# Performance work log

Hardware: AMD Instinct MI355X
Metric: run time of the kernel (lower is better)

Reference implementation:

```python
import jax, jax.numpy as jnp
import numpy as np

N_NODES = 50000
N_EDGES = 800000
IN_F = 129
HID = 32
HEADS = 4
N_CLS = 40
NEG_SLOPE = 0.2
BN_EPS = 1e-5


def setup_inputs() -> dict:
    key = jax.random.key(0)
    ks = jax.random.split(key, 16)
    x = jax.random.normal(ks[0], (N_NODES, IN_F), dtype=jnp.float32)
    edge_index = jax.random.randint(ks[1], (2, N_EDGES), 0, N_NODES, dtype=jnp.int64)
    # BatchNorm1d (eval mode: running stats)
    bn_gamma = jax.random.normal(ks[2], (IN_F,), dtype=jnp.float32) * 0.1 + 1.0
    bn_beta = jax.random.normal(ks[3], (IN_F,), dtype=jnp.float32) * 0.1
    bn_mean = jax.random.normal(ks[4], (IN_F,), dtype=jnp.float32) * 0.1
    bn_var = jax.random.uniform(ks[5], (IN_F,), dtype=jnp.float32, minval=0.5, maxval=1.5)
    # GATConv 1: in=129 -> heads*hid
    s1 = 1.0 / np.sqrt(IN_F)
    W1 = jax.random.uniform(ks[6], (IN_F, HEADS * HID), dtype=jnp.float32, minval=-s1, maxval=s1)
    a1_src = jax.random.uniform(ks[7], (HEADS, HID), dtype=jnp.float32, minval=-s1, maxval=s1)
    a1_dst = jax.random.uniform(ks[8], (HEADS, HID), dtype=jnp.float32, minval=-s1, maxval=s1)
    b1 = jnp.zeros((HEADS * HID,), dtype=jnp.float32)
    # GATConv 2: in=heads*hid -> heads*n_cls (concat=True default)
    in2 = HEADS * HID
    s2 = 1.0 / np.sqrt(in2)
    W2 = jax.random.uniform(ks[9], (in2, HEADS * N_CLS), dtype=jnp.float32, minval=-s2, maxval=s2)
    a2_src = jax.random.uniform(ks[10], (HEADS, N_CLS), dtype=jnp.float32, minval=-s2, maxval=s2)
    a2_dst = jax.random.uniform(ks[11], (HEADS, N_CLS), dtype=jnp.float32, minval=-s2, maxval=s2)
    b2 = jnp.zeros((HEADS * N_CLS,), dtype=jnp.float32)
    return {"x": x, "edge_index": edge_index,
            "bn_gamma": bn_gamma, "bn_beta": bn_beta, "bn_mean": bn_mean, "bn_var": bn_var,
            "W1": W1, "a1_src": a1_src, "a1_dst": a1_dst, "b1": b1,
            "W2": W2, "a2_src": a2_src, "a2_dst": a2_dst, "b2": b2}


def gat_conv(x, W, a_src, a_dst, bias, src, dst, num_nodes, heads, out_ch):
    # h: [N, H, C]
    h = (x @ W).reshape(num_nodes, heads, out_ch)
    alpha_s = jnp.einsum('nhc,hc->nh', h, a_src)   # [N, H]
    alpha_d = jnp.einsum('nhc,hc->nh', h, a_dst)   # [N, H]
    e = alpha_s[src] + alpha_d[dst]                # [E, H]
    e = jnp.where(e > 0, e, NEG_SLOPE * e)         # LeakyReLU
    # segment softmax grouped by destination node
    e_max = jax.ops.segment_max(e, dst, num_segments=num_nodes)
    p = jnp.exp(e - e_max[dst])
    denom = jax.ops.segment_sum(p, dst, num_segments=num_nodes)
    alpha = p / denom[dst]                         # [E, H]
    msg = h[src] * alpha[:, :, None]               # [E, H, C]
    out = jax.ops.segment_sum(msg, dst, num_segments=num_nodes)
    return out.reshape(num_nodes, heads * out_ch) + bias


def reference(x, edge_index, bn_gamma, bn_beta, bn_mean, bn_var,
              W1, a1_src, a1_dst, b1, W2, a2_src, a2_dst, b2):
    N = x.shape[0]
    loops = jnp.arange(N, dtype=edge_index.dtype)
    src = jnp.concatenate([edge_index[0], loops])  # add self loops (PyG default)
    dst = jnp.concatenate([edge_index[1], loops])
    # BatchNorm1d eval; dropout is identity in eval
    h = (x - bn_mean) * jax.lax.rsqrt(bn_var + BN_EPS) * bn_gamma + bn_beta
    h = gat_conv(h, W1, a1_src, a1_dst, b1, src, dst, N, HEADS, HID)
    h = jax.nn.elu(h)
    h = gat_conv(h, W2, a2_src, a2_dst, b2, src, dst, N, HEADS, N_CLS)
    return h
```

## Files before the change

### kernel.cpp

```cpp
#include <hip/hip_runtime.h>

#define N_NODES 50000
#define N_EDGES 800000
#define E_TOT   (N_EDGES + N_NODES)
#define IN_F    129
#define HID     32
#define HEADS   4
#define F1      (HEADS * HID)
#define NCLS    40
#define F2      (HEADS * NCLS)
#define NEG     0.2f
#define BN_EPS  1e-5f
#define PITCH1  132
#define SCAN_NB ((N_NODES + 255) / 256)
#define LOG2E   1.4426950408889634f

__device__ __forceinline__ unsigned pack_bf16(float lo, float hi) {
  unsigned ul = __float_as_uint(lo), uh = __float_as_uint(hi);
  ul = (ul + 0x7FFFu + ((ul >> 16) & 1u)) >> 16;
  uh = (uh + 0x7FFFu + ((uh >> 16) & 1u)) >> 16;
  return ul | (uh << 16);
}

__global__ __launch_bounds__(256) void gemm1_kernel(
    const float* __restrict__ x,
    const float* __restrict__ bng, const float* __restrict__ bnb,
    const float* __restrict__ bnm, const float* __restrict__ bnv,
    const float* __restrict__ W, float* __restrict__ h1) {
  __shared__ float scale[IN_F], shift[IN_F];
  __shared__ float rows[32 * PITCH1];
  int tid = threadIdx.x;
  if (tid < IN_F) {
    float sc = bng[tid] * rsqrtf(bnv[tid] + BN_EPS);
    scale[tid] = sc;
    shift[tid] = bnb[tid] - bnm[tid] * sc;
  }
  __syncthreads();
  int nb = blockIdx.x * 32;
  int nvalid = N_NODES - nb; if (nvalid > 32) nvalid = 32;
  const float* xb = x + (size_t)nb * IN_F;
  int total = nvalid * IN_F;
  for (int i = tid; i < total; i += 256) {
    int r = i / IN_F;
    int c = i - r * IN_F;
    rows[r * PITCH1 + c] = xb[i] * scale[c] + shift[c];
  }
  __syncthreads();
  int wave = tid >> 6, lane = tid & 63;
  int r0 = wave * 8;
  if (r0 >= nvalid) return;
  const float* rp[8];
#pragma unroll
  for (int i = 0; i < 8; i++) {
    int ri = r0 + i; if (ri >= nvalid) ri = nvalid - 1;
    rp[i] = &rows[ri * PITCH1];
  }
  float a0[8] = {}, a1[8] = {};
  for (int k = 0; k < 128; k += 4) {
    float4 xv[8];
#pragma unroll
    for (int i = 0; i < 8; i++) xv[i] = *(const float4*)(rp[i] + k);
    float2 w0 = *(const float2*)&W[(k+0)*F1 + 2*lane];
    float2 w1 = *(const float2*)&W[(k+1)*F1 + 2*lane];
    float2 w2 = *(const float2*)&W[(k+2)*F1 + 2*lane];
    float2 w3 = *(const float2*)&W[(k+3)*F1 + 2*lane];
#pragma unroll
    for (int i = 0; i < 8; i++) {
      a0[i] += xv[i].x*w0.x + xv[i].y*w1.x + xv[i].z*w2.x + xv[i].w*w3.x;
      a1[i] += xv[i].x*w0.y + xv[i].y*w1.y + xv[i].z*w2.y + xv[i].w*w3.y;
    }
  }
  {
    float2 w = *(const float2*)&W[128*F1 + 2*lane];
#pragma unroll
    for (int i = 0; i < 8; i++) { float xk = rp[i][128]; a0[i] += xk*w.x; a1[i] += xk*w.y; }
  }
#pragma unroll
  for (int i = 0; i < 8; i++) {
    if (r0 + i >= nvalid) break;
    size_t n = nb + r0 + i;
    *(float2*)&h1[n * F1 + 2*lane] = make_float2(a0[i], a1[i]);
  }
}

__global__ __launch_bounds__(256) void gemm2_kernel(
    const float* __restrict__ hin, const float* __restrict__ W,
    float* __restrict__ hout, unsigned* __restrict__ h2b) {
  __shared__ float rows[32 * F1];
  int tid = threadIdx.x;
  int nb = blockIdx.x * 32;
  int nvalid = N_NODES - nb; if (nvalid > 32) nvalid = 32;
  const float4* src4 = (const float4*)(hin + (size_t)nb * F1);
  float4* dst4 = (float4*)rows;
  int tot4 = nvalid * (F1 / 4);
  for (int i = tid; i < tot4; i += 256) dst4[i] = src4[i];
  __syncthreads();
  int wave = tid >> 6, lane = tid & 63;
  int r0 = wave * 8;
  if (r0 >= nvalid) return;
  const float* rp[8];
#pragma unroll
  for (int i = 0; i < 8; i++) {
    int ri = r0 + i; if (ri >= nvalid) ri = nvalid - 1;
    rp[i] = &rows[ri * F1];
  }
  bool third = lane < 16;
  float a0[8] = {}, a1[8] = {}, a2[8] = {}, a3[8] = {};
  for (int k = 0; k < F1; k += 4) {
    float4 xv[8];
#pragma unroll
    for (int i = 0; i < 8; i++) xv[i] = *(const float4*)(rp[i] + k);
    float2 w0 = *(const float2*)&W[(k+0)*F2 + 2*lane];
    float2 w1 = *(const float2*)&W[(k+1)*F2 + 2*lane];
    float2 w2 = *(const float2*)&W[(k+2)*F2 + 2*lane];
    float2 w3 = *(const float2*)&W[(k+3)*F2 + 2*lane];
    float2 q0 = third ? *(const float2*)&W[(k+0)*F2 + 128 + 2*lane] : make_float2(0.f,0.f);
    float2 q1 = third ? *(const float2*)&W[(k+1)*F2 + 128 + 2*lane] : make_float2(0.f,0.f);
    float2 q2 = third ? *(const float2*)&W[(k+2)*F2 + 128 + 2*lane] : make_float2(0.f,0.f);
    float2 q3 = third ? *(const float2*)&W[(k+3)*F2 + 128 + 2*lane] : make_float2(0.f,0.f);
#pragma unroll
    for (int i = 0; i < 8; i++) {
      a0[i] += xv[i].x*w0.x + xv[i].y*w1.x + xv[i].z*w2.x + xv[i].w*w3.x;
      a1[i] += xv[i].x*w0.y + xv[i].y*w1.y + xv[i].z*w2.y + xv[i].w*w3.y;
      a2[i] += xv[i].x*q0.x + xv[i].y*q1.x + xv[i].z*q2.x + xv[i].w*q3.x;
      a3[i] += xv[i].x*q0.y + xv[i].y*q1.y + xv[i].z*q2.y + xv[i].w*q3.y;
    }
  }
#pragma unroll
  for (int i = 0; i < 8; i++) {
    if (r0 + i >= nvalid) break;
    size_t n = nb + r0 + i;
    *(float2*)&hout[n * F2 + 2*lane] = make_float2(a0[i], a1[i]);
    h2b[n * (F2/2) + lane] = pack_bf16(a0[i], a1[i]);
    if (third) {
      *(float2*)&hout[n * F2 + 128 + 2*lane] = make_float2(a2[i], a3[i]);
      h2b[n * (F2/2) + 64 + lane] = pack_bf16(a2[i], a3[i]);
    }
  }
}

__global__ __launch_bounds__(256) void alpha1_kernel(
    const float* __restrict__ h1, const float* __restrict__ a_src,
    const float* __restrict__ a_dst, float* __restrict__ as,
    float* __restrict__ ad) {
  int t = blockIdx.x * 256 + threadIdx.x;
  if (t >= N_NODES * HEADS) return;
  int n = t >> 2, h = t & 3;
  const float* hp = h1 + (size_t)n * F1 + h * HID;
  const float* sp = a_src + h * HID;
  const float* dp = a_dst + h * HID;
  float s = 0.f, d = 0.f;
#pragma unroll
  for (int c = 0; c < HID; c++) { float v = hp[c]; s += v * sp[c]; d += v * dp[c]; }
  as[t] = s * LOG2E; ad[t] = d * LOG2E;
}

__global__ __launch_bounds__(256) void alpha2_kernel(
    const float* __restrict__ h2, const float* __restrict__ a_src,
    const float* __restrict__ a_dst, float* __restrict__ as,
    float* __restrict__ ad) {
  int t = blockIdx.x * 256 + threadIdx.x;
  if (t >= N_NODES * HEADS) return;
  int n = t >> 2, h = t & 3;
  const float* hp = h2 + (size_t)n * F2 + h * NCLS;
  const float* sp = a_src + h * NCLS;
  const float* dp = a_dst + h * NCLS;
  float s = 0.f, d = 0.f;
#pragma unroll
  for (int c = 0; c < NCLS; c++) { float v = hp[c]; s += v * sp[c]; d += v * dp[c]; }
  as[t] = s * LOG2E; ad[t] = d * LOG2E;
}

__global__ __launch_bounds__(256) void hist_kernel(
    const int* __restrict__ ei, int* __restrict__ counts) {
  int e = blockIdx.x * 256 + threadIdx.x;
  if (e >= E_TOT) return;
  int dst = (e < N_EDGES) ? ei[N_EDGES + e] : (e - N_EDGES);
  atomicAdd(&counts[dst], 1);
}

__global__ __launch_bounds__(256) void partial_kernel(
    const int* __restrict__ counts, int* __restrict__ bsum) {
  __shared__ int red[4];
  int i = blockIdx.x * 256 + threadIdx.x;
  int v = (i < N_NODES) ? counts[i] : 0;
#pragma unroll
  for (int o = 1; o < 64; o <<= 1) v += __shfl_xor(v, o);
  int lane = threadIdx.x & 63, wave = threadIdx.x >> 6;
  if (lane == 0) red[wave] = v;
  __syncthreads();
  if (threadIdx.x == 0) bsum[blockIdx.x] = red[0] + red[1] + red[2] + red[3];
}

__global__ __launch_bounds__(256) void bscan_kernel(
    const int* __restrict__ bsum, int* __restrict__ bpre) {
  __shared__ int sh[256];
  int t = threadIdx.x;
  int v = (t < SCAN_NB) ? bsum[t] : 0;
  sh[t] = v;
  __syncthreads();
  for (int o = 1; o < 256; o <<= 1) {
    int u = (t >= o) ? sh[t - o] : 0;
    __syncthreads();
    sh[t] += u;
    __syncthreads();
  }
  if (t < SCAN_NB) bpre[t] = sh[t] - v;
}

__global__ __launch_bounds__(256) void scatter_kernel(
    const int* __restrict__ counts, const int* __restrict__ bpre,
    int* __restrict__ offsets, int* __restrict__ fillpos) {
  __shared__ int sh[256];
  int t = threadIdx.x;
  int i = blockIdx.x * 256 + t;
  int v = (i < N_NODES) ? counts[i] : 0;
  sh[t] = v;
  __syncthreads();
  for (int o = 1; o < 256; o <<= 1) {
    int u = (t >= o) ? sh[t - o] : 0;
    __syncthreads();
    sh[t] += u;
    __syncthreads();
  }
  if (i < N_NODES) {
    int excl = bpre[blockIdx.x] + sh[t] - v;
    offsets[i] = excl;
    fillpos[i] = excl;
  }
  if (i == 0) offsets[N_NODES] = E_TOT;
}

__global__ __launch_bounds__(256) void fill_kernel(
    const int* __restrict__ ei, int* __restrict__ fillpos,
    int* __restrict__ csr_src) {
  int e = blockIdx.x * 256 + threadIdx.x;
  if (e >= E_TOT) return;
  int src, dst;
  if (e < N_EDGES) { src = ei[e]; dst = ei[N_EDGES + e]; }
  else { src = dst = e - N_EDGES; }
  int pos = atomicAdd(&fillpos[dst], 1);
  csr_src[pos] = src;
}

__global__ __launch_bounds__(256) void agg1_kernel(
    const float* __restrict__ h1, const float* __restrict__ as,
    const float* __restrict__ ad, const int* __restrict__ off,
    const int* __restrict__ csr, const float* __restrict__ b1,
    float* __restrict__ out) {
  int gw = (blockIdx.x * blockDim.x + threadIdx.x) >> 6;
  int lane = threadIdx.x & 63;
  if (gw >= N_NODES) return;
  int base = off[gw];
  int deg  = off[gw + 1] - base;
  int h = lane & 3;
  int g = lane >> 4;
  float adh = ad[gw * 4 + h];
  float s = 0.f, acc0 = 0.f, acc1 = 0.f;
  int j = 0;
  for (; j + 8 <= deg; j += 8) {
    int sr[8];
#pragma unroll
    for (int u = 0; u < 8; u++) sr[u] = csr[base + j + u];
    float av[8];
#pragma unroll
    for (int u = 0; u < 8; u++) av[u] = as[sr[u]*4 + h];
    float2 xv[8];
#pragma unroll
    for (int u = 0; u < 8; u++)
      xv[u] = *(const float2*)(h1 + (size_t)sr[u] * F1 + 2*lane);
    float w[8];
#pragma unroll
    for (int u = 0; u < 8; u++) {
      float v = av[u] + adh;
      v = fmaxf(v, NEG * v);
      w[u] = __builtin_amdgcn_exp2f(v);
      s += w[u];
    }
#pragma unroll
    for (int u = 0; u < 8; u++) {
      float wg = __shfl(w[u], g);
      acc0 += wg * xv[u].x;
      acc1 += wg * xv[u].y;
    }
  }
  for (; j < deg; j++) {
    int src = csr[base + j];
    float v = as[src*4 + h] + adh;
    v = fmaxf(v, NEG * v);
    float w = __builtin_amdgcn_exp2f(v);
    s += w;
    float2 xv = *(const float2*)(h1 + (size_t)src * F1 + 2*lane);
    float wg = __shfl(w, g);
    acc0 += wg * xv.x;
    acc1 += wg * xv.y;
  }
  float sg = __shfl(s, g);
  float2 bp = *(const float2*)&b1[2*lane];
  float o0 = acc0 / sg + bp.x;
  float o1 = acc1 / sg + bp.y;
  o0 = o0 > 0.f ? o0 : expm1f(o0);
  o1 = o1 > 0.f ? o1 : expm1f(o1);
  *(float2*)&out[(size_t)gw * F1 + 2*lane] = make_float2(o0, o1);
}

__global__ __launch_bounds__(256) void agg2_kernel(
    const unsigned* __restrict__ h2b, const float* __restrict__ as,
    const float* __restrict__ ad, const int* __restrict__ off,
    const int* __restrict__ csr, const float* __restrict__ b2,
    float* __restrict__ out) {
  int gw = (blockIdx.x * blockDim.x + threadIdx.x) >> 6;
  int lane = threadIdx.x & 63;
  if (gw >= N_NODES) return;
  int base = off[gw];
  int deg  = off[gw + 1] - base;
  int h  = lane & 3;
  int gA = lane / 20;
  bool third = lane < 16;
  float adh = ad[gw * 4 + h];
  float s = 0.f, a0 = 0.f, a1 = 0.f, a2 = 0.f, a3 = 0.f;
  int j = 0;
  for (; j + 8 <= deg; j += 8) {
    int sr[8];
#pragma unroll
    for (int u = 0; u < 8; u++) sr[u] = csr[base + j + u];
    float av[8];
#pragma unroll
    for (int u = 0; u < 8; u++) av[u] = as[sr[u]*4 + h];
    unsigned ua[8], ub[8];
#pragma unroll
    for (int u = 0; u < 8; u++) {
      const unsigned* r = h2b + (size_t)sr[u] * (F2/2);
      ua[u] = r[lane];
      ub[u] = third ? r[64 + lane] : 0u;
    }
    float w[8];
#pragma unroll
    for (int u = 0; u < 8; u++) {
      float v = av[u] + adh;
      v = fmaxf(v, NEG * v);
      w[u] = __builtin_amdgcn_exp2f(v);
      s += w[u];
    }
#pragma unroll
    for (int u = 0; u < 8; u++) {
      float wA = __shfl(w[u], gA);
      float w3 = __shfl(w[u], 3);
      a0 += wA * __uint_as_float(ua[u] << 16);
      a1 += wA * __uint_as_float(ua[u] & 0xFFFF0000u);
      a2 += w3 * __uint_as_float(ub[u] << 16);
      a3 += w3 * __uint_as_float(ub[u] & 0xFFFF0000u);
    }
  }
  for (; j < deg; j++) {
    int src = csr[base + j];
    float v = as[src*4 + h] + adh;
    v = fmaxf(v, NEG * v);
    float w = __builtin_amdgcn_exp2f(v);
    s += w;
    const unsigned* r = h2b + (size_t)src * (F2/2);
    unsigned ua = r[lane];
    unsigned ub = third ? r[64 + lane] : 0u;
    float wA = __shfl(w, gA);
    float w3 = __shfl(w, 3);
    a0 += wA * __uint_as_float(ua << 16);
    a1 += wA * __uint_as_float(ua & 0xFFFF0000u);
    a2 += w3 * __uint_as_float(ub << 16);
    a3 += w3 * __uint_as_float(ub & 0xFFFF0000u);
  }
  float sA = __shfl(s, gA), s3 = __shfl(s, 3);
  float2 bp = *(const float2*)&b2[2*lane];
  *(float2*)&out[(size_t)gw * F2 + 2*lane] =
      make_float2(a0/sA + bp.x, a1/sA + bp.y);
  if (third) {
    float2 bq = *(const float2*)&b2[128 + 2*lane];
    *(float2*)&out[(size_t)gw * F2 + 128 + 2*lane] =
        make_float2(a2/s3 + bq.x, a3/s3 + bq.y);
  }
}

extern "C" void kernel_launch(void* const* d_in, const int* in_sizes, int n_in,
                              void* d_out, int out_size, void* d_ws, size_t ws_size,
                              hipStream_t stream) {
  const float* x   = (const float*)d_in[0];
  const int*   ei  = (const int*)d_in[1];
  const float* bng = (const float*)d_in[2];
  const float* bnb = (const float*)d_in[3];
  const float* bnm = (const float*)d_in[4];
  const float* bnv = (const float*)d_in[5];
  const float* W1  = (const float*)d_in[6];
  const float* a1s = (const float*)d_in[7];
  const float* a1d = (const float*)d_in[8];
  const float* b1  = (const float*)d_in[9];
  const float* W2  = (const float*)d_in[10];
  const float* a2s = (const float*)d_in[11];
  const float* a2d = (const float*)d_in[12];
  const float* b2  = (const float*)d_in[13];
  float* out = (float*)d_out;

  char* ws = (char*)d_ws;
  size_t p = 0;
  auto alloc = [&](size_t bytes) -> char* {
    char* r = ws + p;
    p += (bytes + 255) & ~(size_t)255;
    return r;
  };
  float* h1   = (float*)alloc(sizeof(float) * (size_t)N_NODES * F1);
  float* h1a  = (float*)alloc(sizeof(float) * (size_t)N_NODES * F1);
  float* h2   = (float*)alloc(sizeof(float) * (size_t)N_NODES * F2);
  float* as1  = (float*)alloc(sizeof(float) * (size_t)N_NODES * HEADS);
  float* ad1  = (float*)alloc(sizeof(float) * (size_t)N_NODES * HEADS);
  float* as2  = (float*)alloc(sizeof(float) * (size_t)N_NODES * HEADS);
  float* ad2  = (float*)alloc(sizeof(float) * (size_t)N_NODES * HEADS);
  int* counts = (int*)alloc(sizeof(int) * (N_NODES + 1));
  int* offs   = (int*)alloc(sizeof(int) * (N_NODES + 1));
  int* fpos   = (int*)alloc(sizeof(int) * N_NODES);
  int* bsum   = (int*)alloc(sizeof(int) * SCAN_NB);
  int* bpre   = (int*)alloc(sizeof(int) * SCAN_NB);
  int* csr    = (int*)alloc(sizeof(int) * E_TOT);
  unsigned* h2b = (unsigned*)h1;

  hipMemsetAsync(counts, 0, sizeof(int) * (N_NODES + 1), stream);

  hist_kernel<<<(E_TOT + 255) / 256, 256, 0, stream>>>(ei, counts);
  partial_kernel<<<SCAN_NB, 256, 0, stream>>>(counts, bsum);
  bscan_kernel<<<1, 256, 0, stream>>>(bsum, bpre);
  scatter_kernel<<<SCAN_NB, 256, 0, stream>>>(counts, bpre, offs, fpos);
  fill_kernel<<<(E_TOT + 255) / 256, 256, 0, stream>>>(ei, fpos, csr);

  int gblocks = (N_NODES + 31) / 32;
  gemm1_kernel<<<gblocks, 256, 0, stream>>>(x, bng, bnb, bnm, bnv, W1, h1);
  alpha1_kernel<<<(N_NODES * HEADS + 255) / 256, 256, 0, stream>>>(h1, a1s, a1d, as1, ad1);
  agg1_kernel<<<(N_NODES + 3) / 4, 256, 0, stream>>>(h1, as1, ad1, offs, csr, b1, h1a);

  gemm2_kernel<<<gblocks, 256, 0, stream>>>(h1a, W2, h2, h2b);
  alpha2_kernel<<<(N_NODES * HEADS + 255) / 256, 256, 0, stream>>>(h2, a2s, a2d, as2, ad2);
  agg2_kernel<<<(N_NODES + 3) / 4, 256, 0, stream>>>(h2b, as2, ad2, offs, csr, b2, out);
}
```

Baseline: 444.7 us.

## Move both GAT projection GEMMs onto bf16 MFMA with split-precision emulation

Replaces the scalar FP32 FMA GEMMs for both GAT layers with MFMA 16x16x32 bf16 instructions. Each operand is split into high and low bf16 parts and three products are accumulated to approximate FP32 accuracy. A new packing kernel lays out the weights in MFMA fragment order on every call. The 129th input feature is handled as a scalar tail. This trades an extra kernel launch and three times the MFMA work for much higher matrix throughput, at some risk to precision.

```diff
diff --git a/kernel.cpp b/kernel.cpp
--- a/kernel.cpp
+++ b/kernel.cpp
@@ -11,24 +11,60 @@
 #define F2      (HEADS * NCLS)
 #define NEG     0.2f
 #define BN_EPS  1e-5f
-#define PITCH1  132
 #define SCAN_NB ((N_NODES + 255) / 256)
 #define LOG2E   1.4426950408889634f
 
+typedef __attribute__((ext_vector_type(8))) short bf16x8;
+typedef __attribute__((ext_vector_type(4))) float f32x4;
+
+#define P1_ELEMS (8 * 4 * 64 * 8)
+#define P2_ELEMS (10 * 4 * 64 * 8)
+
+__device__ __forceinline__ unsigned short bf16_rne(float f) {
+  unsigned u = __float_as_uint(f);
+  u = (u + 0x7FFFu + ((u >> 16) & 1u)) >> 16;
+  return (unsigned short)u;
+}
+__device__ __forceinline__ float bf16_to_f(unsigned short s) {
+  return __uint_as_float(((unsigned)s) << 16);
+}
 __device__ __forceinline__ unsigned pack_bf16(float lo, float hi) {
-  unsigned ul = __float_as_uint(lo), uh = __float_as_uint(hi);
-  ul = (ul + 0x7FFFu + ((ul >> 16) & 1u)) >> 16;
-  uh = (uh + 0x7FFFu + ((uh >> 16) & 1u)) >> 16;
-  return ul | (uh << 16);
+  return (unsigned)bf16_rne(lo) | ((unsigned)bf16_rne(hi) << 16);
+}
+
+__global__ __launch_bounds__(256) void packw_kernel(
+    const float* __restrict__ W1, const float* __restrict__ W2,
+    unsigned short* __restrict__ p1h, unsigned short* __restrict__ p1l,
+    unsigned short* __restrict__ p2h, unsigned short* __restrict__ p2l) {
+  int e = blockIdx.x * 256 + threadIdx.x;
+  if (e < P1_ELEMS) {
+    int i = e & 7, l = (e >> 3) & 63, c = (e >> 9) & 3, t = e >> 11;
+    int k = c * 32 + (l >> 4) * 8 + i;
+    int col = t * 16 + (l & 15);
+    float v = W1[k * F1 + col];
+    unsigned short hi = bf16_rne(v);
+    p1h[e] = hi;
+    p1l[e] = bf16_rne(v - bf16_to_f(hi));
+  }
+  int e2 = e - P1_ELEMS;
+  if (e2 >= 0 && e2 < P2_ELEMS) {
+    int i = e2 & 7, l = (e2 >> 3) & 63, c = (e2 >> 9) & 3, t = e2 >> 11;
+    int k = c * 32 + (l >> 4) * 8 + i;
+    int col = t * 16 + (l & 15);
+    float v = W2[k * F2 + col];
+    unsigned short hi = bf16_rne(v);
+    p2h[e2] = hi;
+    p2l[e2] = bf16_rne(v - bf16_to_f(hi));
+  }
 }
 
 __global__ __launch_bounds__(256) void gemm1_kernel(
     const float* __restrict__ x,
     const float* __restrict__ bng, const float* __restrict__ bnb,
     const float* __restrict__ bnm, const float* __restrict__ bnv,
-    const float* __restrict__ W, float* __restrict__ h1) {
+    const unsigned short* __restrict__ p1h, const unsigned short* __restrict__ p1l,
+    const float* __restrict__ W1, float* __restrict__ h1) {
   __shared__ float scale[IN_F], shift[IN_F];
-  __shared__ float rows[32 * PITCH1];
   int tid = threadIdx.x;
   if (tid < IN_F) {
     float sc = bng[tid] * rsqrtf(bnv[tid] + BN_EPS);
@@ -36,105 +72,102 @@
     shift[tid] = bnb[tid] - bnm[tid] * sc;
   }
   __syncthreads();
-  int nb = blockIdx.x * 32;
-  int nvalid = N_NODES - nb; if (nvalid > 32) nvalid = 32;
-  const float* xb = x + (size_t)nb * IN_F;
-  int total = nvalid * IN_F;
-  for (int i = tid; i < total; i += 256) {
-    int r = i / IN_F;
-    int c = i - r * IN_F;
-    rows[r * PITCH1 + c] = xb[i] * scale[c] + shift[c];
-  }
-  __syncthreads();
-  int wave = tid >> 6, lane = tid & 63;
-  int r0 = wave * 8;
-  if (r0 >= nvalid) return;
-  const float* rp[8];
-#pragma unroll
-  for (int i = 0; i < 8; i++) {
-    int ri = r0 + i; if (ri >= nvalid) ri = nvalid - 1;
-    rp[i] = &rows[ri * PITCH1];
-  }
-  float a0[8] = {}, a1[8] = {};
-  for (int k = 0; k < 128; k += 4) {
-    float4 xv[8];
-#pragma unroll
-    for (int i = 0; i < 8; i++) xv[i] = *(const float4*)(rp[i] + k);
-    float2 w0 = *(const float2*)&W[(k+0)*F1 + 2*lane];
-    float2 w1 = *(const float2*)&W[(k+1)*F1 + 2*lane];
-    float2 w2 = *(const float2*)&W[(k+2)*F1 + 2*lane];
-    float2 w3 = *(const float2*)&W[(k+3)*F1 + 2*lane];
+  int lane = tid & 63, wave = tid >> 6;
+  int row0 = blockIdx.x * 64 + wave * 16;
+  if (row0 >= N_NODES) return;
+  int arow = row0 + (lane & 15);
+  int arow_c = arow < N_NODES ? arow : N_NODES - 1;
+  int kb = (lane >> 4) * 8;
+  const float* xr = x + (size_t)arow_c * IN_F;
+  bf16x8 ah[4], al[4];
+#pragma unroll
+  for (int c = 0; c < 4; c++) {
+    int k0 = c * 32 + kb;
 #pragma unroll
     for (int i = 0; i < 8; i++) {
-      a0[i] += xv[i].x*w0.x + xv[i].y*w1.x + xv[i].z*w2.x + xv[i].w*w3.x;
-      a1[i] += xv[i].x*w0.y + xv[i].y*w1.y + xv[i].z*w2.y + xv[i].w*w3.y;
-    }
-  }
-  {
-    float2 w = *(const float2*)&W[128*F1 + 2*lane];
-#pragma unroll
-    for (int i = 0; i < 8; i++) { float xk = rp[i][128]; a0[i] += xk*w.x; a1[i] += xk*w.y; }
-  }
-#pragma unroll
-  for (int i = 0; i < 8; i++) {
-    if (r0 + i >= nvalid) break;
-    size_t n = nb + r0 + i;
-    *(float2*)&h1[n * F1 + 2*lane] = make_float2(a0[i], a1[i]);
+      float a = xr[k0 + i] * scale[k0 + i] + shift[k0 + i];
+      unsigned short hi = bf16_rne(a);
+      ah[c][i] = (short)hi;
+      al[c][i] = (short)bf16_rne(a - bf16_to_f(hi));
+    }
+  }
+  int crow_base = row0 + (lane >> 4) * 4;
+  float atail[4];
+#pragma unroll
+  for (int r = 0; r < 4; r++) {
+    int rr = crow_base + r;
+    rr = rr < N_NODES ? rr : N_NODES - 1;
+    atail[r] = x[(size_t)rr * IN_F + 128] * scale[128] + shift[128];
+  }
+  int col0 = lane & 15;
+  for (int t = 0; t < 8; t++) {
+    f32x4 acc = {0.f, 0.f, 0.f, 0.f};
+#pragma unroll
+    for (int c = 0; c < 4; c++) {
+      bf16x8 bh = *(const bf16x8*)(p1h + ((t * 4 + c) * 64 + lane) * 8);
+      bf16x8 bl = *(const bf16x8*)(p1l + ((t * 4 + c) * 64 + lane) * 8);
+      acc = __builtin_amdgcn_mfma_f32_16x16x32_bf16(ah[c], bh, acc, 0, 0, 0);
+      acc = __builtin_amdgcn_mfma_f32_16x16x32_bf16(al[c], bh, acc, 0, 0, 0);
+      acc = __builtin_amdgcn_mfma_f32_16x16x32_bf16(ah[c], bl, acc, 0, 0, 0);
+    }
+    int col = t * 16 + col0;
+    float wtail = W1[128 * F1 + col];
+#pragma unroll
+    for (int r = 0; r < 4; r++) {
+      int rr = crow_base + r;
+      if (rr < N_NODES)
+        h1[(size_t)rr * F1 + col] = acc[r] + atail[r] * wtail;
+    }
   }
 }
 
 __global__ __launch_bounds__(256) void gemm2_kernel(
-    const float* __restrict__ hin, const float* __restrict__ W,
-    float* __restrict__ hout, unsigned* __restrict__ h2b) {
-  __shared__ float rows[32 * F1];
+    const float* __restrict__ hin,
+    const unsigned short* __restrict__ p2h, const unsigned short* __restrict__ p2l,
+    float* __restrict__ h2, unsigned* __restrict__ h2b) {
   int tid = threadIdx.x;
-  int nb = blockIdx.x * 32;
-  int nvalid = N_NODES - nb; if (nvalid > 32) nvalid = 32;
-  const float4* src4 = (const float4*)(hin + (size_t)nb * F1);
-  float4* dst4 = (float4*)rows;
-  int tot4 = nvalid * (F1 / 4);
-  for (int i = tid; i < tot4; i += 256) dst4[i] = src4[i];
-  __syncthreads();
-  int wave = tid >> 6, lane = tid & 63;
-  int r0 = wave * 8;
-  if (r0 >= nvalid) return;
-  const float* rp[8];
-#pragma unroll
-  for (int i = 0; i < 8; i++) {
-    int ri = r0 + i; if (ri >= nvalid) ri = nvalid - 1;
-    rp[i] = &rows[ri * F1];
-  }
-  bool third = lane < 16;
-  float a0[8] = {}, a1[8] = {}, a2[8] = {}, a3[8] = {};
-  for (int k = 0; k < F1; k += 4) {
-    float4 xv[8];
-#pragma unroll
-    for (int i = 0; i < 8; i++) xv[i] = *(const float4*)(rp[i] + k);
-    float2 w0 = *(const float2*)&W[(k+0)*F2 + 2*lane];
-    float2 w1 = *(const float2*)&W[(k+1)*F2 + 2*lane];
-    float2 w2 = *(const float2*)&W[(k+2)*F2 + 2*lane];
-    float2 w3 = *(const float2*)&W[(k+3)*F2 + 2*lane];
-    float2 q0 = third ? *(const float2*)&W[(k+0)*F2 + 128 + 2*lane] : make_float2(0.f,0.f);
-    float2 q1 = third ? *(const float2*)&W[(k+1)*F2 + 128 + 2*lane] : make_float2(0.f,0.f);
-    float2 q2 = third ? *(const float2*)&W[(k+2)*F2 + 128 + 2*lane] : make_float2(0.f,0.f);
-    float2 q3 = third ? *(const float2*)&W[(k+3)*F2 + 128 + 2*lane] : make_float2(0.f,0.f);
+  int lane = tid & 63, wave = tid >> 6;
+  int row0 = blockIdx.x * 64 + wave * 16;
+  if (row0 >= N_NODES) return;
+  int arow = row0 + (lane & 15);
+  int arow_c = arow < N_NODES ? arow : N_NODES - 1;
+  int kb = (lane >> 4) * 8;
+  const float* hr = hin + (size_t)arow_c * F1;
+  bf16x8 ah[4], al[4];
+#pragma unroll
+  for (int c = 0; c < 4; c++) {
+    float4 v0 = *(const float4*)(hr + c * 32 + kb);
+    float4 v1 = *(const float4*)(hr + c * 32 + kb + 4);
+    float av[8] = {v0.x, v0.y, v0.z, v0.w, v1.x, v1.y, v1.z, v1.w};
 #pragma unroll
     for (int i = 0; i < 8; i++) {
-      a0[i] += xv[i].x*w0.x + xv[i].y*w1.x + xv[i].z*w2.x + xv[i].w*w3.x;
-      a1[i] += xv[i].x*w0.y + xv[i].y*w1.y + xv[i].z*w2.y + xv[i].w*w3.y;
-      a2[i] += xv[i].x*q0.x + xv[i].y*q1.x + xv[i].z*q2.x + xv[i].w*q3.x;
-      a3[i] += xv[i].x*q0.y + xv[i].y*q1.y + xv[i].z*q2.y + xv[i].w*q3.y;
-    }
-  }
-#pragma unroll
-  for (int i = 0; i < 8; i++) {
-    if (r0 + i >= nvalid) break;
-    size_t n = nb + r0 + i;
-    *(float2*)&hout[n * F2 + 2*lane] = make_float2(a0[i], a1[i]);
-    h2b[n * (F2/2) + lane] = pack_bf16(a0[i], a1[i]);
-    if (third) {
-      *(float2*)&hout[n * F2 + 128 + 2*lane] = make_float2(a2[i], a3[i]);
-      h2b[n * (F2/2) + 64 + lane] = pack_bf16(a2[i], a3[i]);
+      unsigned short hi = bf16_rne(av[i]);
+      ah[c][i] = (short)hi;
+      al[c][i] = (short)bf16_rne(av[i] - bf16_to_f(hi));
+    }
+  }
+  int crow_base = row0 + (lane >> 4) * 4;
+  int col0 = lane & 15;
+  for (int t = 0; t < 10; t++) {
+    f32x4 acc = {0.f, 0.f, 0.f, 0.f};
+#pragma unroll
+    for (int c = 0; c < 4; c++) {
+      bf16x8 bh = *(const bf16x8*)(p2h + ((t * 4 + c) * 64 + lane) * 8);
+      bf16x8 bl = *(const bf16x8*)(p2l + ((t * 4 + c) * 64 + lane) * 8);
+      acc = __builtin_amdgcn_mfma_f32_16x16x32_bf16(ah[c], bh, acc, 0, 0, 0);
+      acc = __builtin_amdgcn_mfma_f32_16x16x32_bf16(al[c], bh, acc, 0, 0, 0);
+      acc = __builtin_amdgcn_mfma_f32_16x16x32_bf16(ah[c], bl, acc, 0, 0, 0);
+    }
+    int col = t * 16 + col0;
+#pragma unroll
+    for (int r = 0; r < 4; r++) {
+      int rr = crow_base + r;
+      float odd = __shfl(acc[r], lane + 1);
+      if (rr < N_NODES) {
+        h2[(size_t)rr * F2 + col] = acc[r];
+        if ((lane & 1) == 0)
+          h2b[(size_t)rr * (F2 / 2) + (col >> 1)] = pack_bf16(acc[r], odd);
+      }
     }
   }
 }
@@ -418,9 +451,16 @@
   int* bsum   = (int*)alloc(sizeof(int) * SCAN_NB);
   int* bpre   = (int*)alloc(sizeof(int) * SCAN_NB);
   int* csr    = (int*)alloc(sizeof(int) * E_TOT);
+  unsigned short* p1h = (unsigned short*)alloc(sizeof(unsigned short) * P1_ELEMS);
+  unsigned short* p1l = (unsigned short*)alloc(sizeof(unsigned short) * P1_ELEMS);
+  unsigned short* p2h = (unsigned short*)alloc(sizeof(unsigned short) * P2_ELEMS);
+  unsigned short* p2l = (unsigned short*)alloc(sizeof(unsigned short) * P2_ELEMS);
   unsigned* h2b = (unsigned*)h1;
 
   hipMemsetAsync(counts, 0, sizeof(int) * (N_NODES + 1), stream);
+
+  packw_kernel<<<(P1_ELEMS + P2_ELEMS + 255) / 256, 256, 0, stream>>>(
+      W1, W2, p1h, p1l, p2h, p2l);
 
   hist_kernel<<<(E_TOT + 255) / 256, 256, 0, stream>>>(ei, counts);
   partial_kernel<<<SCAN_NB, 256, 0, stream>>>(counts, bsum);
@@ -428,12 +468,12 @@
   scatter_kernel<<<SCAN_NB, 256, 0, stream>>>(counts, bpre, offs, fpos);
   fill_kernel<<<(E_TOT + 255) / 256, 256, 0, stream>>>(ei, fpos, csr);
 
-  int gblocks = (N_NODES + 31) / 32;
-  gemm1_kernel<<<gblocks, 256, 0, stream>>>(x, bng, bnb, bnm, bnv, W1, h1);
+  int gblocks = (N_NODES + 63) / 64;
+  gemm1_kernel<<<gblocks, 256, 0, stream>>>(x, bng, bnb, bnm, bnv, p1h, p1l, W1, h1);
   alpha1_kernel<<<(N_NODES * HEADS + 255) / 256, 256, 0, stream>>>(h1, a1s, a1d, as1, ad1);
   agg1_kernel<<<(N_NODES + 3) / 4, 256, 0, stream>>>(h1, as1, ad1, offs, csr, b1, h1a);
 
-  gemm2_kernel<<<gblocks, 256, 0, stream>>>(h1a, W2, h2, h2b);
+  gemm2_kernel<<<gblocks, 256, 0, stream>>>(h1a, p2h, p2l, h2, h2b);
   alpha2_kernel<<<(N_NODES * HEADS + 255) / 256, 256, 0, stream>>>(h2, a2s, a2d, as2, ad2);
   agg2_kernel<<<(N_NODES + 3) / 4, 256, 0, stream>>>(h2b, as2, ad2, offs, csr, b2, out);
 }
```

Result: faster. 382.6 us (-14.0%).
